# Optimization experiments

Measured on AMD Instinct MI355X. Metric: run time of the kernel, lower is better.

The kernel has to match this reference:

```python
import jax, jax.numpy as jnp
import numpy as np

N, IN_F, OUT_F, HID, R = 384, 64, 4, 32, 16
EPS = 1e-5
CUT_LO, CUT_HI = 0.0, 5.0


def _expnormal_smearing(dist):
    # dist: [N, N, 1] -> [N, N, R]; torchmd-net ExpNormalSmearing with cosine cutoff
    alpha = 5.0 / (CUT_HI - CUT_LO)
    start = float(np.exp(-CUT_HI + CUT_LO))
    means = jnp.linspace(start, 1.0, R, dtype=dist.dtype)          # [R]
    beta = (2.0 / R * (1.0 - start)) ** -2
    cutoff = 0.5 * (jnp.cos(dist * jnp.pi / CUT_HI) + 1.0) * (dist < CUT_HI)
    return cutoff * jnp.exp(-beta * (jnp.exp(alpha * (CUT_LO - dist)) - means) ** 2)


def setup_inputs() -> dict:
    key = jax.random.key(0)
    k = jax.random.split(key, 5)
    x = jax.random.normal(k[0], (N, 3), dtype=jnp.float32) * 2.0        # node positions
    h = jax.random.normal(k[1], (N, IN_F), dtype=jnp.float32)           # node features
    W_fc = jax.random.normal(k[2], (2 * R * HID, IN_F), dtype=jnp.float32) / np.sqrt(IN_F)
    W_sum = jax.random.normal(k[3], (2 * OUT_F * R, HID), dtype=jnp.float32) / np.sqrt(HID)
    b_sum = jnp.zeros((2 * OUT_F * R,), dtype=jnp.float32)
    return {"x": x, "h": h, "W_fc": W_fc, "W_sum": W_sum, "b_sum": b_sum}


def reference(x, h, W_fc, W_sum, b_sum):
    # --- TransductiveParameter.forward ---
    hp = h @ W_fc.T                                  # [N, 2*R*H]
    hp = hp[:, None, :] + hp[None, :, :]             # [N, N, 2*R*H]
    K, Q = jnp.split(hp, 2, axis=-1)                 # each [N, N, R*H]
    K = K.reshape(N, N, R, HID)
    Q = Q.reshape(N, N, R, HID)

    # --- JunmaiLayer.forward ---
    dx = x[:, None, :] - x[None, :, :]               # [N, N, 3]
    nsq = jnp.sum(dx * dx, axis=-1, keepdims=True) + EPS
    nrm = jnp.sqrt(nsq)                              # [N, N, 1]
    dxn = dx / nsq                                   # [N, N, 3]
    smear = _expnormal_smearing(nrm)                 # [N, N, R]
    basis = smear[..., None] * dxn[..., None, :]     # [N, N, R, 3]

    bk = jnp.einsum('mnrb,mnrc->mcb', basis, K)      # [N, H, 3]
    bq = jnp.einsum('mnrb,mnrc->mcb', basis, Q)      # [N, H, 3]
    att = jnp.sum(bk * bq, axis=-1)                  # [N, H]
    out = jax.nn.silu(att) @ W_sum.T + b_sum         # [N, 2*out*R]

    hh = out.reshape(N, R, 2 * OUT_F)
    hh = hh[:, None, :, :] + hh[None, :, :, :]       # [N, N, R, 2*out]
    K2, Q2 = jnp.split(hh, 2, axis=-1)               # each [N, N, R, out]
    return (K2, Q2)
```

## Files before the change

### kernel.cpp

```cpp
#include <hip/hip_runtime.h>
#include <math.h>

#define NN 384
#define IN_F 64
#define HID 32
#define RR 16
#define HP_W 1024
#define EPSF 1e-5f
#define CHUNK 48
#define NCHUNK 8
#define MT 2

__global__ __launch_bounds__(256) void k_hp(const float* __restrict__ h,
                                            const float* __restrict__ Wfc,
                                            float* __restrict__ hpT) {
    int m = blockIdx.x;
    __shared__ float4 hs4[IN_F / 4];
    int tid = threadIdx.x;
    if (tid < IN_F / 4) hs4[tid] = ((const float4*)(h + m * IN_F))[tid];
    __syncthreads();
    const float4* W4 = (const float4*)Wfc;
    for (int jj = 0; jj < 4; ++jj) {
        int j = tid + 256 * jj;
        const float4* row = W4 + (size_t)j * (IN_F / 4);
        float acc = 0.f;
#pragma unroll
        for (int k = 0; k < IN_F / 4; ++k) {
            float4 w = row[k];
            float4 hv = hs4[k];
            acc += w.x * hv.x + w.y * hv.y + w.z * hv.z + w.w * hv.w;
        }
        int kq = j >> 9, rc = j & 511, r = rc >> 5, c = rc & 31;
        hpT[(size_t)m * HP_W + kq * 512 + c * 16 + r] = acc;
    }
}

__global__ __launch_bounds__(256) void k_mid(const float* __restrict__ x,
                                             const float* __restrict__ hpT,
                                             float* __restrict__ pbk,
                                             float* __restrict__ pS,
                                             float beta, float start) {
    const int ch = blockIdx.x;
    const int m0 = blockIdx.y * MT;
    const int n0 = ch * CHUNK;
    const int tid = threadIdx.x;

    __shared__ float smear_s[MT][CHUNK][16];
    __shared__ float dxn_s[MT][CHUNK][3];
    __shared__ float red_s[4][MT][64][3];

    for (int it = tid; it < MT * CHUNK * 16; it += 256) {
        int mi = it / (CHUNK * 16);
        int rest = it % (CHUNK * 16);
        int np = rest >> 4, r = rest & 15;
        int m = m0 + mi, n = n0 + np;
        float d0 = x[m * 3 + 0] - x[n * 3 + 0];
        float d1 = x[m * 3 + 1] - x[n * 3 + 1];
        float d2 = x[m * 3 + 2] - x[n * 3 + 2];
        float nsq = d0 * d0 + d1 * d1 + d2 * d2 + EPSF;
        float dist = sqrtf(nsq);
        float cut = (dist < 5.0f) ? 0.5f * (__cosf(dist * 0.62831853071795864769f) + 1.0f) : 0.0f;
        float en = __expf(-dist);
        float mean_r = start + (1.0f - start) * ((float)r * (1.0f / 15.0f));
        float dmr = en - mean_r;
        smear_s[mi][np][r] = cut * __expf(-beta * dmr * dmr);
        if (r < 3) dxn_s[mi][np][r] = ((r == 0) ? d0 : ((r == 1) ? d1 : d2)) / nsq;
    }
    __syncthreads();

    const int g = tid >> 6, kq = (tid >> 5) & 1, c = tid & 31;
    float a00 = 0.f, a01 = 0.f, a02 = 0.f, a10 = 0.f, a11 = 0.f, a12 = 0.f;
    const float* hpbase = hpT + (size_t)(n0 + g * 12) * HP_W + kq * 512 + c * 16;
    for (int ni = 0; ni < 12; ++ni) {
        const int np = g * 12 + ni;
        const float4* hp4 = (const float4*)(hpbase + (size_t)ni * HP_W);
        float4 h0 = hp4[0], h1 = hp4[1], h2 = hp4[2], h3 = hp4[3];
        {
            const float4* sm4 = (const float4*)smear_s[0][np];
            float4 s0 = sm4[0], s1 = sm4[1], s2 = sm4[2], s3 = sm4[3];
            float P = h0.x * s0.x + h0.y * s0.y + h0.z * s0.z + h0.w * s0.w
                    + h1.x * s1.x + h1.y * s1.y + h1.z * s1.z + h1.w * s1.w
                    + h2.x * s2.x + h2.y * s2.y + h2.z * s2.z + h2.w * s2.w
                    + h3.x * s3.x + h3.y * s3.y + h3.z * s3.z + h3.w * s3.w;
            a00 += P * dxn_s[0][np][0];
            a01 += P * dxn_s[0][np][1];
            a02 += P * dxn_s[0][np][2];
        }
        {
            const float4* sm4 = (const float4*)smear_s[1][np];
            float4 s0 = sm4[0], s1 = sm4[1], s2 = sm4[2], s3 = sm4[3];
            float P = h0.x * s0.x + h0.y * s0.y + h0.z * s0.z + h0.w * s0.w
                    + h1.x * s1.x + h1.y * s1.y + h1.z * s1.z + h1.w * s1.w
                    + h2.x * s2.x + h2.y * s2.y + h2.z * s2.z + h2.w * s2.w
                    + h3.x * s3.x + h3.y * s3.y + h3.z * s3.z + h3.w * s3.w;
            a10 += P * dxn_s[1][np][0];
            a11 += P * dxn_s[1][np][1];
            a12 += P * dxn_s[1][np][2];
        }
    }
    red_s[g][0][kq * 32 + c][0] = a00;
    red_s[g][0][kq * 32 + c][1] = a01;
    red_s[g][0][kq * 32 + c][2] = a02;
    red_s[g][1][kq * 32 + c][0] = a10;
    red_s[g][1][kq * 32 + c][1] = a11;
    red_s[g][1][kq * 32 + c][2] = a12;

    float accS = 0.f;
    int smi = 0, ss = 0;
    if (tid < MT * 48) {
        smi = tid / 48; ss = tid % 48;
        const int r = ss / 3, b = ss % 3;
        for (int np = 0; np < CHUNK; ++np)
            accS += smear_s[smi][np][r] * dxn_s[smi][np][b];
    }
    __syncthreads();

    for (int it = tid; it < MT * 192; it += 256) {
        int mi = it / 192, j = it % 192;
        int kq2 = j / 96, b2 = (j % 96) / 32, c2 = j % 32;
        float v = red_s[0][mi][kq2 * 32 + c2][b2] + red_s[1][mi][kq2 * 32 + c2][b2]
                + red_s[2][mi][kq2 * 32 + c2][b2] + red_s[3][mi][kq2 * 32 + c2][b2];
        pbk[((size_t)(m0 + mi) * NCHUNK + ch) * 192 + j] = v;
    }
    if (tid < MT * 48)
        pS[((size_t)(m0 + smi) * NCHUNK + ch) * 48 + ss] = accS;
}

__global__ __launch_bounds__(256) void k_combine(const float* __restrict__ hpT,
                                                 const float* __restrict__ Wsum,
                                                 const float* __restrict__ bsum,
                                                 const float* __restrict__ pbk,
                                                 const float* __restrict__ pS,
                                                 float* __restrict__ outv) {
    const int m = blockIdx.x;
    const int tid = threadIdx.x;
    __shared__ float S_s[16][3];
    __shared__ float bkq_s[2][HID][3];
    __shared__ float silu_s[HID];

    float v = 0.f;
    if (tid < 192) {
        for (int chn = 0; chn < NCHUNK; ++chn)
            v += pbk[((size_t)m * NCHUNK + chn) * 192 + tid];
    } else if (tid < 240) {
        int s = tid - 192;
        float a = 0.f;
        for (int chn = 0; chn < NCHUNK; ++chn)
            a += pS[((size_t)m * NCHUNK + chn) * 48 + s];
        S_s[s / 3][s % 3] = a;
    }
    __syncthreads();
    if (tid < 192) {
        const int kq = tid / 96, b = (tid % 96) / 32, cc = tid % 32;
        const float4* hb = (const float4*)(hpT + (size_t)m * HP_W + kq * 512 + cc * 16);
        float4 h0 = hb[0], h1 = hb[1], h2 = hb[2], h3 = hb[3];
        v += h0.x * S_s[0][b] + h0.y * S_s[1][b] + h0.z * S_s[2][b] + h0.w * S_s[3][b]
           + h1.x * S_s[4][b] + h1.y * S_s[5][b] + h1.z * S_s[6][b] + h1.w * S_s[7][b]
           + h2.x * S_s[8][b] + h2.y * S_s[9][b] + h2.z * S_s[10][b] + h2.w * S_s[11][b]
           + h3.x * S_s[12][b] + h3.y * S_s[13][b] + h3.z * S_s[14][b] + h3.w * S_s[15][b];
        bkq_s[kq][cc][b] = v;
    }
    __syncthreads();
    if (tid < HID) {
        float a = bkq_s[0][tid][0] * bkq_s[1][tid][0]
                + bkq_s[0][tid][1] * bkq_s[1][tid][1]
                + bkq_s[0][tid][2] * bkq_s[1][tid][2];
        silu_s[tid] = a / (1.0f + __expf(-a));
    }
    __syncthreads();
    if (tid < 128) {
        float acc = bsum[tid];
        const float* wr = Wsum + tid * HID;
#pragma unroll
        for (int c2 = 0; c2 < HID; ++c2) acc += wr[c2] * silu_s[c2];
        outv[(size_t)m * 128 + tid] = acc;
    }
}

__global__ __launch_bounds__(256) void k_expand(const float* __restrict__ outv,
                                                float* __restrict__ out) {
    const int bid = blockIdx.x;
    const int m = bid / 24;
    const int n0 = (bid % 24) * 16;
    const int tid = threadIdx.x;
    __shared__ float4 om[32];
    if (tid < 32) om[tid] = ((const float4*)(outv + (size_t)m * 128))[tid];
    __syncthreads();
    const int ni = tid >> 4;
    const int r = tid & 15;
    const int n = n0 + ni;
    const float4* on = (const float4*)(outv + (size_t)n * 128);
    float4 a0 = om[2 * r], a1 = om[2 * r + 1];
    float4 b0 = on[2 * r], b1 = on[2 * r + 1];
    float4 k2 = make_float4(a0.x + b0.x, a0.y + b0.y, a0.z + b0.z, a0.w + b0.w);
    float4 q2 = make_float4(a1.x + b1.x, a1.y + b1.y, a1.z + b1.z, a1.w + b1.w);
    float4* o4 = (float4*)out;
    const size_t idx = ((size_t)(m * NN + n) * RR + r);
    o4[idx] = k2;
    o4[(size_t)NN * NN * RR + idx] = q2;
}

extern "C" void kernel_launch(void* const* d_in, const int* in_sizes, int n_in,
                              void* d_out, int out_size, void* d_ws, size_t ws_size,
                              hipStream_t stream) {
    const float* x    = (const float*)d_in[0];
    const float* h    = (const float*)d_in[1];
    const float* Wfc  = (const float*)d_in[2];
    const float* Wsum = (const float*)d_in[3];
    const float* bsum = (const float*)d_in[4];
    float* out = (float*)d_out;

    float* hpT  = (float*)d_ws;
    float* outv = hpT + (size_t)NN * HP_W;
    float* pbk  = outv + (size_t)NN * 128;
    float* pS   = pbk + (size_t)NN * NCHUNK * 192;

    double startd = exp(-5.0);
    double rd = (2.0 / 16.0) * (1.0 - startd);
    float beta = (float)(1.0 / (rd * rd));
    float start = (float)startd;

    k_hp<<<NN, 256, 0, stream>>>(h, Wfc, hpT);
    k_mid<<<dim3(NCHUNK, NN / MT), 256, 0, stream>>>(x, hpT, pbk, pS, beta, start);
    k_combine<<<NN, 256, 0, stream>>>(hpT, Wsum, bsum, pbk, pS, outv);
    k_expand<<<NN * 24, 256, 0, stream>>>(outv, out);
}
```

Baseline: 70.48 us.

## Fuse combine into mid kernel via atomic accumulation and last-block finalize

```diff
diff --git a/kernel.cpp b/kernel.cpp
--- a/kernel.cpp
+++ b/kernel.cpp
@@ -10,13 +10,26 @@
 #define CHUNK 48
 #define NCHUNK 8
 #define MT 2
+#define NGROUP (NN / MT)
+
+typedef float f4 __attribute__((ext_vector_type(4)));
+
 
 __global__ __launch_bounds__(256) void k_hp(const float* __restrict__ h,
                                             const float* __restrict__ Wfc,
-                                            float* __restrict__ hpT) {
+                                            float* __restrict__ hpT,
+                                            float* __restrict__ bk_acc,
+                                            float* __restrict__ S_acc,
+                                            unsigned* __restrict__ counter) {
     int m = blockIdx.x;
+    int tid = threadIdx.x;
+    {
+        int gid = m * 256 + tid;
+        if (gid < NN * 192) bk_acc[gid] = 0.f;
+        else if (gid < NN * 192 + NN * 48) S_acc[gid - NN * 192] = 0.f;
+        else if (gid < NN * 192 + NN * 48 + NGROUP) counter[gid - NN * 192 - NN * 48] = 0u;
+    }
     __shared__ float4 hs4[IN_F / 4];
-    int tid = threadIdx.x;
     if (tid < IN_F / 4) hs4[tid] = ((const float4*)(h + m * IN_F))[tid];
     __syncthreads();
     const float4* W4 = (const float4*)Wfc;
@@ -37,17 +50,26 @@
 
 __global__ __launch_bounds__(256) void k_mid(const float* __restrict__ x,
                                              const float* __restrict__ hpT,
-                                             float* __restrict__ pbk,
-                                             float* __restrict__ pS,
+                                             const float* __restrict__ Wsum,
+                                             const float* __restrict__ bsum,
+                                             float* __restrict__ bk_acc,
+                                             float* __restrict__ S_acc,
+                                             unsigned* __restrict__ counter,
+                                             float* __restrict__ outv,
                                              float beta, float start) {
     const int ch = blockIdx.x;
-    const int m0 = blockIdx.y * MT;
+    const int mg = blockIdx.y;
+    const int m0 = mg * MT;
     const int n0 = ch * CHUNK;
     const int tid = threadIdx.x;
 
     __shared__ float smear_s[MT][CHUNK][16];
     __shared__ float dxn_s[MT][CHUNK][3];
     __shared__ float red_s[4][MT][64][3];
+    __shared__ float S_s[16][3];
+    __shared__ float bkq_s[2][HID][3];
+    __shared__ float silu_s[HID];
+    __shared__ int last_s;
 
     for (int it = tid; it < MT * CHUNK * 16; it += 256) {
         int mi = it / (CHUNK * 16);
@@ -106,9 +128,8 @@
     red_s[g][1][kq * 32 + c][2] = a12;
 
     float accS = 0.f;
-    int smi = 0, ss = 0;
     if (tid < MT * 48) {
-        smi = tid / 48; ss = tid % 48;
+        const int smi = tid / 48, ss = tid % 48;
         const int r = ss / 3, b = ss % 3;
         for (int np = 0; np < CHUNK; ++np)
             accS += smear_s[smi][np][r] * dxn_s[smi][np][b];
@@ -120,60 +141,50 @@
         int kq2 = j / 96, b2 = (j % 96) / 32, c2 = j % 32;
         float v = red_s[0][mi][kq2 * 32 + c2][b2] + red_s[1][mi][kq2 * 32 + c2][b2]
                 + red_s[2][mi][kq2 * 32 + c2][b2] + red_s[3][mi][kq2 * 32 + c2][b2];
-        pbk[((size_t)(m0 + mi) * NCHUNK + ch) * 192 + j] = v;
+        atomicAdd(&bk_acc[(size_t)(m0 + mi) * 192 + j], v);
     }
     if (tid < MT * 48)
-        pS[((size_t)(m0 + smi) * NCHUNK + ch) * 48 + ss] = accS;
-}
-
-__global__ __launch_bounds__(256) void k_combine(const float* __restrict__ hpT,
-                                                 const float* __restrict__ Wsum,
-                                                 const float* __restrict__ bsum,
-                                                 const float* __restrict__ pbk,
-                                                 const float* __restrict__ pS,
-                                                 float* __restrict__ outv) {
-    const int m = blockIdx.x;
-    const int tid = threadIdx.x;
-    __shared__ float S_s[16][3];
-    __shared__ float bkq_s[2][HID][3];
-    __shared__ float silu_s[HID];
-
-    float v = 0.f;
-    if (tid < 192) {
-        for (int chn = 0; chn < NCHUNK; ++chn)
-            v += pbk[((size_t)m * NCHUNK + chn) * 192 + tid];
-    } else if (tid < 240) {
-        int s = tid - 192;
-        float a = 0.f;
-        for (int chn = 0; chn < NCHUNK; ++chn)
-            a += pS[((size_t)m * NCHUNK + chn) * 48 + s];
-        S_s[s / 3][s % 3] = a;
-    }
-    __syncthreads();
-    if (tid < 192) {
-        const int kq = tid / 96, b = (tid % 96) / 32, cc = tid % 32;
-        const float4* hb = (const float4*)(hpT + (size_t)m * HP_W + kq * 512 + cc * 16);
-        float4 h0 = hb[0], h1 = hb[1], h2 = hb[2], h3 = hb[3];
-        v += h0.x * S_s[0][b] + h0.y * S_s[1][b] + h0.z * S_s[2][b] + h0.w * S_s[3][b]
-           + h1.x * S_s[4][b] + h1.y * S_s[5][b] + h1.z * S_s[6][b] + h1.w * S_s[7][b]
-           + h2.x * S_s[8][b] + h2.y * S_s[9][b] + h2.z * S_s[10][b] + h2.w * S_s[11][b]
-           + h3.x * S_s[12][b] + h3.y * S_s[13][b] + h3.z * S_s[14][b] + h3.w * S_s[15][b];
-        bkq_s[kq][cc][b] = v;
-    }
-    __syncthreads();
-    if (tid < HID) {
-        float a = bkq_s[0][tid][0] * bkq_s[1][tid][0]
-                + bkq_s[0][tid][1] * bkq_s[1][tid][1]
-                + bkq_s[0][tid][2] * bkq_s[1][tid][2];
-        silu_s[tid] = a / (1.0f + __expf(-a));
-    }
-    __syncthreads();
-    if (tid < 128) {
-        float acc = bsum[tid];
-        const float* wr = Wsum + tid * HID;
+        atomicAdd(&S_acc[(size_t)(m0 + tid / 48) * 48 + (tid % 48)], accS);
+
+    __threadfence();
+    if (tid == 0) last_s = (atomicAdd(&counter[mg], 1u) == NCHUNK - 1) ? 1 : 0;
+    __syncthreads();
+    if (!last_s) return;
+
+    for (int mi = 0; mi < MT; ++mi) {
+        const int m = m0 + mi;
+        if (tid < 48) {
+            float a = atomicAdd(&S_acc[(size_t)m * 48 + tid], 0.f);
+            S_s[tid / 3][tid % 3] = a;
+        }
+        __syncthreads();
+        if (tid < 192) {
+            const int kqe = tid / 96, b = (tid % 96) / 32, cc = tid % 32;
+            float v = atomicAdd(&bk_acc[(size_t)m * 192 + tid], 0.f);
+            const float4* hb = (const float4*)(hpT + (size_t)m * HP_W + kqe * 512 + cc * 16);
+            float4 h0 = hb[0], h1 = hb[1], h2 = hb[2], h3 = hb[3];
+            v += h0.x * S_s[0][b] + h0.y * S_s[1][b] + h0.z * S_s[2][b] + h0.w * S_s[3][b]
+               + h1.x * S_s[4][b] + h1.y * S_s[5][b] + h1.z * S_s[6][b] + h1.w * S_s[7][b]
+               + h2.x * S_s[8][b] + h2.y * S_s[9][b] + h2.z * S_s[10][b] + h2.w * S_s[11][b]
+               + h3.x * S_s[12][b] + h3.y * S_s[13][b] + h3.z * S_s[14][b] + h3.w * S_s[15][b];
+            bkq_s[kqe][cc][b] = v;
+        }
+        __syncthreads();
+        if (tid < HID) {
+            float a = bkq_s[0][tid][0] * bkq_s[1][tid][0]
+                    + bkq_s[0][tid][1] * bkq_s[1][tid][1]
+                    + bkq_s[0][tid][2] * bkq_s[1][tid][2];
+            silu_s[tid] = a / (1.0f + __expf(-a));
+        }
+        __syncthreads();
+        if (tid < 128) {
+            float acc = bsum[tid];
+            const float* wr = Wsum + tid * HID;
 #pragma unroll
-        for (int c2 = 0; c2 < HID; ++c2) acc += wr[c2] * silu_s[c2];
-        outv[(size_t)m * 128 + tid] = acc;
+            for (int c2 = 0; c2 < HID; ++c2) acc += wr[c2] * silu_s[c2];
+            outv[(size_t)m * 128 + tid] = acc;
+        }
+        __syncthreads();
     }
 }
 
@@ -192,12 +203,12 @@
     const float4* on = (const float4*)(outv + (size_t)n * 128);
     float4 a0 = om[2 * r], a1 = om[2 * r + 1];
     float4 b0 = on[2 * r], b1 = on[2 * r + 1];
-    float4 k2 = make_float4(a0.x + b0.x, a0.y + b0.y, a0.z + b0.z, a0.w + b0.w);
-    float4 q2 = make_float4(a1.x + b1.x, a1.y + b1.y, a1.z + b1.z, a1.w + b1.w);
-    float4* o4 = (float4*)out;
+    f4 k2 = {a0.x + b0.x, a0.y + b0.y, a0.z + b0.z, a0.w + b0.w};
+    f4 q2 = {a1.x + b1.x, a1.y + b1.y, a1.z + b1.z, a1.w + b1.w};
+    f4* o4 = (f4*)out;
     const size_t idx = ((size_t)(m * NN + n) * RR + r);
-    o4[idx] = k2;
-    o4[(size_t)NN * NN * RR + idx] = q2;
+    __builtin_nontemporal_store(k2, o4 + idx);
+    __builtin_nontemporal_store(q2, o4 + (size_t)NN * NN * RR + idx);
 }
 
 extern "C" void kernel_launch(void* const* d_in, const int* in_sizes, int n_in,
@@ -210,18 +221,19 @@
     const float* bsum = (const float*)d_in[4];
     float* out = (float*)d_out;
 
-    float* hpT  = (float*)d_ws;
-    float* outv = hpT + (size_t)NN * HP_W;
-    float* pbk  = outv + (size_t)NN * 128;
-    float* pS   = pbk + (size_t)NN * NCHUNK * 192;
+    float* hpT   = (float*)d_ws;
+    float* outv  = hpT + (size_t)NN * HP_W;
+    float* bk_acc = outv + (size_t)NN * 128;
+    float* S_acc  = bk_acc + (size_t)NN * 192;
+    unsigned* counter = (unsigned*)(S_acc + (size_t)NN * 48);
 
     double startd = exp(-5.0);
     double rd = (2.0 / 16.0) * (1.0 - startd);
     float beta = (float)(1.0 / (rd * rd));
     float start = (float)startd;
 
-    k_hp<<<NN, 256, 0, stream>>>(h, Wfc, hpT);
-    k_mid<<<dim3(NCHUNK, NN / MT), 256, 0, stream>>>(x, hpT, pbk, pS, beta, start);
-    k_combine<<<NN, 256, 0, stream>>>(hpT, Wsum, bsum, pbk, pS, outv);
+    k_hp<<<NN, 256, 0, stream>>>(h, Wfc, hpT, bk_acc, S_acc, counter);
+    k_mid<<<dim3(NCHUNK, NGROUP), 256, 0, stream>>>(x, hpT, Wsum, bsum,
+                                                    bk_acc, S_acc, counter, outv, beta, start);
     k_expand<<<NN * 24, 256, 0, stream>>>(outv, out);
 }
```

Result: slower. 179.8 us (+155.1%).

## Fuse mid and combine kernels into one 1024-thread block per node pair

Applied to the files above, without the earlier changes.

```diff
diff --git a/kernel.cpp b/kernel.cpp
--- a/kernel.cpp
+++ b/kernel.cpp
@@ -7,16 +7,15 @@
 #define RR 16
 #define HP_W 1024
 #define EPSF 1e-5f
-#define CHUNK 48
-#define NCHUNK 8
-#define MT 2
+
+typedef float f4 __attribute__((ext_vector_type(4)));
 
 __global__ __launch_bounds__(256) void k_hp(const float* __restrict__ h,
                                             const float* __restrict__ Wfc,
                                             float* __restrict__ hpT) {
     int m = blockIdx.x;
+    int tid = threadIdx.x;
     __shared__ float4 hs4[IN_F / 4];
-    int tid = threadIdx.x;
     if (tid < IN_F / 4) hs4[tid] = ((const float4*)(h + m * IN_F))[tid];
     __syncthreads();
     const float4* W4 = (const float4*)Wfc;
@@ -35,28 +34,33 @@
     }
 }
 
-__global__ __launch_bounds__(256) void k_mid(const float* __restrict__ x,
-                                             const float* __restrict__ hpT,
-                                             float* __restrict__ pbk,
-                                             float* __restrict__ pS,
-                                             float beta, float start) {
-    const int ch = blockIdx.x;
-    const int m0 = blockIdx.y * MT;
-    const int n0 = ch * CHUNK;
+__global__ __launch_bounds__(1024) void k_midc(const float* __restrict__ x,
+                                               const float* __restrict__ hpT,
+                                               const float* __restrict__ Wsum,
+                                               const float* __restrict__ bsum,
+                                               float* __restrict__ outv,
+                                               float beta, float start) {
+    const int m0 = blockIdx.x * 2;
     const int tid = threadIdx.x;
 
-    __shared__ float smear_s[MT][CHUNK][16];
-    __shared__ float dxn_s[MT][CHUNK][3];
-    __shared__ float red_s[4][MT][64][3];
-
-    for (int it = tid; it < MT * CHUNK * 16; it += 256) {
-        int mi = it / (CHUNK * 16);
-        int rest = it % (CHUNK * 16);
+    __shared__ float smear_s[2][NN][16];
+    __shared__ float dxn_s[2][NN][3];
+    __shared__ float bk_lds[2][64][4];
+    __shared__ float S_lds[2][64];
+    __shared__ float bkq_s[2][2][32][4];
+    __shared__ float silu_s[2][32];
+
+    if (tid < 512) ((float*)bk_lds)[tid] = 0.f;
+    else if (tid < 640) ((float*)S_lds)[tid - 512] = 0.f;
+
+    for (int it = tid; it < 2 * NN * 16; it += 1024) {
+        int mi = it / (NN * 16);
+        int rest = it - mi * (NN * 16);
         int np = rest >> 4, r = rest & 15;
-        int m = m0 + mi, n = n0 + np;
-        float d0 = x[m * 3 + 0] - x[n * 3 + 0];
-        float d1 = x[m * 3 + 1] - x[n * 3 + 1];
-        float d2 = x[m * 3 + 2] - x[n * 3 + 2];
+        int m = m0 + mi;
+        float d0 = x[m * 3 + 0] - x[np * 3 + 0];
+        float d1 = x[m * 3 + 1] - x[np * 3 + 1];
+        float d2 = x[m * 3 + 2] - x[np * 3 + 2];
         float nsq = d0 * d0 + d1 * d1 + d2 * d2 + EPSF;
         float dist = sqrtf(nsq);
         float cut = (dist < 5.0f) ? 0.5f * (__cosf(dist * 0.62831853071795864769f) + 1.0f) : 0.0f;
@@ -70,10 +74,10 @@
 
     const int g = tid >> 6, kq = (tid >> 5) & 1, c = tid & 31;
     float a00 = 0.f, a01 = 0.f, a02 = 0.f, a10 = 0.f, a11 = 0.f, a12 = 0.f;
-    const float* hpbase = hpT + (size_t)(n0 + g * 12) * HP_W + kq * 512 + c * 16;
-    for (int ni = 0; ni < 12; ++ni) {
-        const int np = g * 12 + ni;
-        const float4* hp4 = (const float4*)(hpbase + (size_t)ni * HP_W);
+    const float* hpb = hpT + (size_t)(g * 24) * HP_W + kq * 512 + c * 16;
+    for (int ni = 0; ni < 24; ++ni) {
+        const int np = g * 24 + ni;
+        const float4* hp4 = (const float4*)(hpb + (size_t)ni * HP_W);
         float4 h0 = hp4[0], h1 = hp4[1], h2 = hp4[2], h3 = hp4[3];
         {
             const float4* sm4 = (const float4*)smear_s[0][np];
@@ -98,82 +102,55 @@
             a12 += P * dxn_s[1][np][2];
         }
     }
-    red_s[g][0][kq * 32 + c][0] = a00;
-    red_s[g][0][kq * 32 + c][1] = a01;
-    red_s[g][0][kq * 32 + c][2] = a02;
-    red_s[g][1][kq * 32 + c][0] = a10;
-    red_s[g][1][kq * 32 + c][1] = a11;
-    red_s[g][1][kq * 32 + c][2] = a12;
-
-    float accS = 0.f;
-    int smi = 0, ss = 0;
-    if (tid < MT * 48) {
-        smi = tid / 48; ss = tid % 48;
-        const int r = ss / 3, b = ss % 3;
-        for (int np = 0; np < CHUNK; ++np)
-            accS += smear_s[smi][np][r] * dxn_s[smi][np][b];
-    }
-    __syncthreads();
-
-    for (int it = tid; it < MT * 192; it += 256) {
-        int mi = it / 192, j = it % 192;
-        int kq2 = j / 96, b2 = (j % 96) / 32, c2 = j % 32;
-        float v = red_s[0][mi][kq2 * 32 + c2][b2] + red_s[1][mi][kq2 * 32 + c2][b2]
-                + red_s[2][mi][kq2 * 32 + c2][b2] + red_s[3][mi][kq2 * 32 + c2][b2];
-        pbk[((size_t)(m0 + mi) * NCHUNK + ch) * 192 + j] = v;
-    }
-    if (tid < MT * 48)
-        pS[((size_t)(m0 + smi) * NCHUNK + ch) * 48 + ss] = accS;
-}
-
-__global__ __launch_bounds__(256) void k_combine(const float* __restrict__ hpT,
-                                                 const float* __restrict__ Wsum,
-                                                 const float* __restrict__ bsum,
-                                                 const float* __restrict__ pbk,
-                                                 const float* __restrict__ pS,
-                                                 float* __restrict__ outv) {
-    const int m = blockIdx.x;
-    const int tid = threadIdx.x;
-    __shared__ float S_s[16][3];
-    __shared__ float bkq_s[2][HID][3];
-    __shared__ float silu_s[HID];
-
-    float v = 0.f;
-    if (tid < 192) {
-        for (int chn = 0; chn < NCHUNK; ++chn)
-            v += pbk[((size_t)m * NCHUNK + chn) * 192 + tid];
-    } else if (tid < 240) {
-        int s = tid - 192;
-        float a = 0.f;
-        for (int chn = 0; chn < NCHUNK; ++chn)
-            a += pS[((size_t)m * NCHUNK + chn) * 48 + s];
-        S_s[s / 3][s % 3] = a;
-    }
-    __syncthreads();
-    if (tid < 192) {
-        const int kq = tid / 96, b = (tid % 96) / 32, cc = tid % 32;
-        const float4* hb = (const float4*)(hpT + (size_t)m * HP_W + kq * 512 + cc * 16);
+    atomicAdd(&bk_lds[0][kq * 32 + c][0], a00);
+    atomicAdd(&bk_lds[0][kq * 32 + c][1], a01);
+    atomicAdd(&bk_lds[0][kq * 32 + c][2], a02);
+    atomicAdd(&bk_lds[1][kq * 32 + c][0], a10);
+    atomicAdd(&bk_lds[1][kq * 32 + c][1], a11);
+    atomicAdd(&bk_lds[1][kq * 32 + c][2], a12);
+
+    const int lane = tid & 63;
+    if (lane < 48) {
+        const int rr = lane / 3, bb = lane - rr * 3;
+        float s0 = 0.f, s1 = 0.f;
+        for (int ni = 0; ni < 24; ++ni) {
+            const int np = g * 24 + ni;
+            s0 += smear_s[0][np][rr] * dxn_s[0][np][bb];
+            s1 += smear_s[1][np][rr] * dxn_s[1][np][bb];
+        }
+        atomicAdd(&S_lds[0][lane], s0);
+        atomicAdd(&S_lds[1][lane], s1);
+    }
+    __syncthreads();
+
+    const int half = tid >> 9, trem = tid & 511;
+    const int m = m0 + half;
+    if (trem < 192) {
+        const int kqe = trem / 96, b = (trem % 96) / 32, cc = trem % 32;
+        float v = bk_lds[half][kqe * 32 + cc][b];
+        const float4* hb = (const float4*)(hpT + (size_t)m * HP_W + kqe * 512 + cc * 16);
         float4 h0 = hb[0], h1 = hb[1], h2 = hb[2], h3 = hb[3];
-        v += h0.x * S_s[0][b] + h0.y * S_s[1][b] + h0.z * S_s[2][b] + h0.w * S_s[3][b]
-           + h1.x * S_s[4][b] + h1.y * S_s[5][b] + h1.z * S_s[6][b] + h1.w * S_s[7][b]
-           + h2.x * S_s[8][b] + h2.y * S_s[9][b] + h2.z * S_s[10][b] + h2.w * S_s[11][b]
-           + h3.x * S_s[12][b] + h3.y * S_s[13][b] + h3.z * S_s[14][b] + h3.w * S_s[15][b];
-        bkq_s[kq][cc][b] = v;
-    }
-    __syncthreads();
-    if (tid < HID) {
-        float a = bkq_s[0][tid][0] * bkq_s[1][tid][0]
-                + bkq_s[0][tid][1] * bkq_s[1][tid][1]
-                + bkq_s[0][tid][2] * bkq_s[1][tid][2];
-        silu_s[tid] = a / (1.0f + __expf(-a));
-    }
-    __syncthreads();
-    if (tid < 128) {
-        float acc = bsum[tid];
-        const float* wr = Wsum + tid * HID;
+        const float* Sh = S_lds[half];
+        v += h0.x * Sh[0 * 3 + b]  + h0.y * Sh[1 * 3 + b]  + h0.z * Sh[2 * 3 + b]  + h0.w * Sh[3 * 3 + b]
+           + h1.x * Sh[4 * 3 + b]  + h1.y * Sh[5 * 3 + b]  + h1.z * Sh[6 * 3 + b]  + h1.w * Sh[7 * 3 + b]
+           + h2.x * Sh[8 * 3 + b]  + h2.y * Sh[9 * 3 + b]  + h2.z * Sh[10 * 3 + b] + h2.w * Sh[11 * 3 + b]
+           + h3.x * Sh[12 * 3 + b] + h3.y * Sh[13 * 3 + b] + h3.z * Sh[14 * 3 + b] + h3.w * Sh[15 * 3 + b];
+        bkq_s[half][kqe][cc][b] = v;
+    }
+    __syncthreads();
+    if (trem < 32) {
+        float aa = bkq_s[half][0][trem][0] * bkq_s[half][1][trem][0]
+                 + bkq_s[half][0][trem][1] * bkq_s[half][1][trem][1]
+                 + bkq_s[half][0][trem][2] * bkq_s[half][1][trem][2];
+        silu_s[half][trem] = aa / (1.0f + __expf(-aa));
+    }
+    __syncthreads();
+    if (trem < 128) {
+        float acc = bsum[trem];
+        const float* wr = Wsum + trem * HID;
 #pragma unroll
-        for (int c2 = 0; c2 < HID; ++c2) acc += wr[c2] * silu_s[c2];
-        outv[(size_t)m * 128 + tid] = acc;
+        for (int c2 = 0; c2 < HID; ++c2) acc += wr[c2] * silu_s[half][c2];
+        outv[(size_t)m * 128 + trem] = acc;
     }
 }
 
@@ -192,12 +169,12 @@
     const float4* on = (const float4*)(outv + (size_t)n * 128);
     float4 a0 = om[2 * r], a1 = om[2 * r + 1];
     float4 b0 = on[2 * r], b1 = on[2 * r + 1];
-    float4 k2 = make_float4(a0.x + b0.x, a0.y + b0.y, a0.z + b0.z, a0.w + b0.w);
-    float4 q2 = make_float4(a1.x + b1.x, a1.y + b1.y, a1.z + b1.z, a1.w + b1.w);
-    float4* o4 = (float4*)out;
+    f4 k2 = {a0.x + b0.x, a0.y + b0.y, a0.z + b0.z, a0.w + b0.w};
+    f4 q2 = {a1.x + b1.x, a1.y + b1.y, a1.z + b1.z, a1.w + b1.w};
+    f4* o4 = (f4*)out;
     const size_t idx = ((size_t)(m * NN + n) * RR + r);
-    o4[idx] = k2;
-    o4[(size_t)NN * NN * RR + idx] = q2;
+    __builtin_nontemporal_store(k2, o4 + idx);
+    __builtin_nontemporal_store(q2, o4 + (size_t)NN * NN * RR + idx);
 }
 
 extern "C" void kernel_launch(void* const* d_in, const int* in_sizes, int n_in,
@@ -212,8 +189,6 @@
 
     float* hpT  = (float*)d_ws;
     float* outv = hpT + (size_t)NN * HP_W;
-    float* pbk  = outv + (size_t)NN * 128;
-    float* pS   = pbk + (size_t)NN * NCHUNK * 192;
 
     double startd = exp(-5.0);
     double rd = (2.0 / 16.0) * (1.0 - startd);
@@ -221,7 +196,6 @@
     float start = (float)startd;
 
     k_hp<<<NN, 256, 0, stream>>>(h, Wfc, hpT);
-    k_mid<<<dim3(NCHUNK, NN / MT), 256, 0, stream>>>(x, hpT, pbk, pS, beta, start);
-    k_combine<<<NN, 256, 0, stream>>>(hpT, Wsum, bsum, pbk, pS, outv);
+    k_midc<<<NN / 2, 1024, 0, stream>>>(x, hpT, Wsum, bsum, outv, beta, start);
     k_expand<<<NN * 24, 256, 0, stream>>>(outv, out);
 }
```

Result: slower. 95.45 us (+35.4%).

## Fuse combine and pairwise expand into one tiled kernel with nontemporal stores

Applied to the files above, without the earlier changes.

```diff
diff --git a/kernel.cpp b/kernel.cpp
--- a/kernel.cpp
+++ b/kernel.cpp
@@ -11,12 +11,14 @@
 #define NCHUNK 8
 #define MT 2
 
+typedef float f4 __attribute__((ext_vector_type(4)));
+
 __global__ __launch_bounds__(256) void k_hp(const float* __restrict__ h,
                                             const float* __restrict__ Wfc,
                                             float* __restrict__ hpT) {
     int m = blockIdx.x;
+    int tid = threadIdx.x;
     __shared__ float4 hs4[IN_F / 4];
-    int tid = threadIdx.x;
     if (tid < IN_F / 4) hs4[tid] = ((const float4*)(h + m * IN_F))[tid];
     __syncthreads();
     const float4* W4 = (const float4*)Wfc;
@@ -126,78 +128,103 @@
         pS[((size_t)(m0 + smi) * NCHUNK + ch) * 48 + ss] = accS;
 }
 
-__global__ __launch_bounds__(256) void k_combine(const float* __restrict__ hpT,
+__global__ __launch_bounds__(256) void k_expfuse(const float* __restrict__ hpT,
                                                  const float* __restrict__ Wsum,
                                                  const float* __restrict__ bsum,
                                                  const float* __restrict__ pbk,
                                                  const float* __restrict__ pS,
-                                                 float* __restrict__ outv) {
-    const int m = blockIdx.x;
+                                                 float* __restrict__ out) {
+    const int bj = blockIdx.x, bi = blockIdx.y;
     const int tid = threadIdx.x;
-    __shared__ float S_s[16][3];
-    __shared__ float bkq_s[2][HID][3];
-    __shared__ float silu_s[HID];
-
-    float v = 0.f;
-    if (tid < 192) {
-        for (int chn = 0; chn < NCHUNK; ++chn)
-            v += pbk[((size_t)m * NCHUNK + chn) * 192 + tid];
-    } else if (tid < 240) {
-        int s = tid - 192;
+
+    __shared__ float S_lds[32][48];
+    __shared__ float silu_lds[32][32];
+    __shared__ float outr[32][132];
+
+#pragma unroll
+    for (int k = 0; k < 6; ++k) {
+        int it = tid + k * 256;
+        int row = it / 48, s = it - row * 48;
+        int mg = (row < 16) ? (bi * 16 + row) : (bj * 16 + row - 16);
         float a = 0.f;
-        for (int chn = 0; chn < NCHUNK; ++chn)
-            a += pS[((size_t)m * NCHUNK + chn) * 48 + s];
-        S_s[s / 3][s % 3] = a;
-    }
-    __syncthreads();
-    if (tid < 192) {
-        const int kq = tid / 96, b = (tid % 96) / 32, cc = tid % 32;
-        const float4* hb = (const float4*)(hpT + (size_t)m * HP_W + kq * 512 + cc * 16);
-        float4 h0 = hb[0], h1 = hb[1], h2 = hb[2], h3 = hb[3];
-        v += h0.x * S_s[0][b] + h0.y * S_s[1][b] + h0.z * S_s[2][b] + h0.w * S_s[3][b]
-           + h1.x * S_s[4][b] + h1.y * S_s[5][b] + h1.z * S_s[6][b] + h1.w * S_s[7][b]
-           + h2.x * S_s[8][b] + h2.y * S_s[9][b] + h2.z * S_s[10][b] + h2.w * S_s[11][b]
-           + h3.x * S_s[12][b] + h3.y * S_s[13][b] + h3.z * S_s[14][b] + h3.w * S_s[15][b];
-        bkq_s[kq][cc][b] = v;
-    }
-    __syncthreads();
-    if (tid < HID) {
-        float a = bkq_s[0][tid][0] * bkq_s[1][tid][0]
-                + bkq_s[0][tid][1] * bkq_s[1][tid][1]
-                + bkq_s[0][tid][2] * bkq_s[1][tid][2];
-        silu_s[tid] = a / (1.0f + __expf(-a));
-    }
-    __syncthreads();
-    if (tid < 128) {
-        float acc = bsum[tid];
-        const float* wr = Wsum + tid * HID;
-#pragma unroll
-        for (int c2 = 0; c2 < HID; ++c2) acc += wr[c2] * silu_s[c2];
-        outv[(size_t)m * 128 + tid] = acc;
-    }
-}
-
-__global__ __launch_bounds__(256) void k_expand(const float* __restrict__ outv,
-                                                float* __restrict__ out) {
-    const int bid = blockIdx.x;
-    const int m = bid / 24;
-    const int n0 = (bid % 24) * 16;
-    const int tid = threadIdx.x;
-    __shared__ float4 om[32];
-    if (tid < 32) om[tid] = ((const float4*)(outv + (size_t)m * 128))[tid];
-    __syncthreads();
-    const int ni = tid >> 4;
-    const int r = tid & 15;
-    const int n = n0 + ni;
-    const float4* on = (const float4*)(outv + (size_t)n * 128);
-    float4 a0 = om[2 * r], a1 = om[2 * r + 1];
-    float4 b0 = on[2 * r], b1 = on[2 * r + 1];
-    float4 k2 = make_float4(a0.x + b0.x, a0.y + b0.y, a0.z + b0.z, a0.w + b0.w);
-    float4 q2 = make_float4(a1.x + b1.x, a1.y + b1.y, a1.z + b1.z, a1.w + b1.w);
-    float4* o4 = (float4*)out;
-    const size_t idx = ((size_t)(m * NN + n) * RR + r);
-    o4[idx] = k2;
-    o4[(size_t)NN * NN * RR + idx] = q2;
+#pragma unroll
+        for (int ch = 0; ch < NCHUNK; ++ch) a += pS[((size_t)mg * NCHUNK + ch) * 48 + s];
+        S_lds[row][s] = a;
+    }
+    __syncthreads();
+
+#pragma unroll
+    for (int k = 0; k < 4; ++k) {
+        int it = tid + k * 256;
+        int row = it >> 5, c = it & 31;
+        int mg = (row < 16) ? (bi * 16 + row) : (bj * 16 + row - 16);
+        const float* Sh = S_lds[row];
+        float bk[2][3];
+#pragma unroll
+        for (int kq = 0; kq < 2; ++kq) {
+            float b0 = 0.f, b1 = 0.f, b2 = 0.f;
+#pragma unroll
+            for (int ch = 0; ch < NCHUNK; ++ch) {
+                const float* pb = pbk + ((size_t)mg * NCHUNK + ch) * 192 + kq * 96 + c;
+                b0 += pb[0]; b1 += pb[32]; b2 += pb[64];
+            }
+            const float4* hb = (const float4*)(hpT + (size_t)mg * HP_W + kq * 512 + c * 16);
+            float4 h0 = hb[0], h1 = hb[1], h2 = hb[2], h3 = hb[3];
+            bk[kq][0] = b0; bk[kq][1] = b1; bk[kq][2] = b2;
+#pragma unroll
+            for (int b = 0; b < 3; ++b) {
+                bk[kq][b] += h0.x * Sh[0 + b]  + h0.y * Sh[3 + b]  + h0.z * Sh[6 + b]  + h0.w * Sh[9 + b]
+                           + h1.x * Sh[12 + b] + h1.y * Sh[15 + b] + h1.z * Sh[18 + b] + h1.w * Sh[21 + b]
+                           + h2.x * Sh[24 + b] + h2.y * Sh[27 + b] + h2.z * Sh[30 + b] + h2.w * Sh[33 + b]
+                           + h3.x * Sh[36 + b] + h3.y * Sh[39 + b] + h3.z * Sh[42 + b] + h3.w * Sh[45 + b];
+            }
+        }
+        float att = bk[0][0] * bk[1][0] + bk[0][1] * bk[1][1] + bk[0][2] * bk[1][2];
+        silu_lds[row][c] = att / (1.0f + __expf(-att));
+    }
+    __syncthreads();
+
+    {
+        const int j = tid & 127, half = tid >> 7;
+        float4 w[8];
+        const float4* wr = (const float4*)(Wsum + j * HID);
+#pragma unroll
+        for (int k = 0; k < 8; ++k) w[k] = wr[k];
+        const float bj_ = bsum[j];
+#pragma unroll
+        for (int rr = 0; rr < 16; ++rr) {
+            const int row = half * 16 + rr;
+            const float4* s4 = (const float4*)silu_lds[row];
+            float acc = bj_;
+#pragma unroll
+            for (int k = 0; k < 8; ++k) {
+                float4 sv = s4[k];
+                acc += w[k].x * sv.x + w[k].y * sv.y + w[k].z * sv.z + w[k].w * sv.w;
+            }
+            outr[row][j] = acc;
+        }
+    }
+    __syncthreads();
+
+    {
+        const int w = tid >> 6, lane = tid & 63, p = lane >> 4, r = lane & 15;
+        f4* o4 = (f4*)out;
+#pragma unroll
+        for (int it2 = 0; it2 < 16; ++it2) {
+            const int mi = w * 4 + (it2 >> 2);
+            const int nj = (it2 & 3) * 4 + p;
+            const int m = bi * 16 + mi, n = bj * 16 + nj;
+            const float4* rm4 = (const float4*)outr[mi];
+            const float4* rn4 = (const float4*)outr[16 + nj];
+            float4 a0 = rm4[2 * r], a1 = rm4[2 * r + 1];
+            float4 b0 = rn4[2 * r], b1 = rn4[2 * r + 1];
+            f4 k2 = {a0.x + b0.x, a0.y + b0.y, a0.z + b0.z, a0.w + b0.w};
+            f4 q2 = {a1.x + b1.x, a1.y + b1.y, a1.z + b1.z, a1.w + b1.w};
+            const size_t idx = ((size_t)(m * NN + n) * RR + r);
+            __builtin_nontemporal_store(k2, o4 + idx);
+            __builtin_nontemporal_store(q2, o4 + (size_t)NN * NN * RR + idx);
+        }
+    }
 }
 
 extern "C" void kernel_launch(void* const* d_in, const int* in_sizes, int n_in,
@@ -210,10 +237,9 @@
     const float* bsum = (const float*)d_in[4];
     float* out = (float*)d_out;
 
-    float* hpT  = (float*)d_ws;
-    float* outv = hpT + (size_t)NN * HP_W;
-    float* pbk  = outv + (size_t)NN * 128;
-    float* pS   = pbk + (size_t)NN * NCHUNK * 192;
+    float* hpT = (float*)d_ws;
+    float* pbk = hpT + (size_t)NN * HP_W;
+    float* pS  = pbk + (size_t)NN * NCHUNK * 192;
 
     double startd = exp(-5.0);
     double rd = (2.0 / 16.0) * (1.0 - startd);
@@ -222,6 +248,5 @@
 
     k_hp<<<NN, 256, 0, stream>>>(h, Wfc, hpT);
     k_mid<<<dim3(NCHUNK, NN / MT), 256, 0, stream>>>(x, hpT, pbk, pS, beta, start);
-    k_combine<<<NN, 256, 0, stream>>>(hpT, Wsum, bsum, pbk, pS, outv);
-    k_expand<<<NN * 24, 256, 0, stream>>>(outv, out);
-}
+    k_expfuse<<<dim3(24, 24), 256, 0, stream>>>(hpT, Wsum, bsum, pbk, pS, out);
+}
```

New measurement: 85.44 us. 1.21x slower.
